# Performance work log

Measured on AMD Instinct MI355X. Metric: run time of the kernel, lower is better.

Reference implementation:

```python
import jax, jax.numpy as jnp
import numpy as np

B, L, IN_DIM, D_MODEL = 4, 1024, 128, 256
MDIM = 2 * D_MODEL          # mamba_dim = 512 (must equal 2*d_model for shape consistency)
NL = 4                      # mamba_layers
DIN = 2 * MDIM              # d_inner (expand=2)
NST = 16                    # d_state
DTR = MDIM // 16            # dt_rank = 32
KC = 4                      # d_conv
EPS = 1e-5

# sinusoidal positional encoding buffer (deterministic)
_pos = np.arange(L, dtype=np.float32)[:, None]
_div = np.exp(np.arange(0, MDIM, 2, dtype=np.float32) * (-np.log(10000.0) / MDIM))
_pe = np.zeros((L, MDIM), dtype=np.float32)
_pe[:, 0::2] = np.sin(_pos * _div)
_pe[:, 1::2] = np.cos(_pos * _div)
PE = jnp.asarray(_pe)


def setup_inputs() -> dict:
    key = jax.random.key(0)
    ks = iter(jax.random.split(key, 64))
    rn = lambda shape, s=0.02: jax.random.normal(next(ks), shape, jnp.float32) * s
    inp = {
        "x": jax.random.normal(next(ks), (B, L, IN_DIM), jnp.float32),
        "rtg": jax.random.normal(next(ks), (B, L, 1), jnp.float32),
        "state_emb_w": rn((D_MODEL, IN_DIM)), "state_emb_b": jnp.zeros((D_MODEL,)),
        "reward_emb_w": rn((D_MODEL, 1)), "reward_emb_b": jnp.zeros((D_MODEL,)),
        "ln_w": jnp.ones((MDIM,)), "ln_b": jnp.zeros((MDIM,)),
        "in_proj_w": rn((NL, 2 * DIN, MDIM)),
        "conv_w": rn((NL, DIN, KC), 0.1), "conv_b": jnp.zeros((NL, DIN)),
        "x_proj_w": rn((NL, DTR + 2 * NST, DIN)),
        "dt_proj_w": rn((NL, DIN, DTR), 0.1), "dt_proj_b": jnp.full((NL, DIN), -2.0),
        "A_log": jnp.tile(jnp.log(jnp.arange(1, NST + 1, dtype=jnp.float32)), (NL, DIN, 1)),
        "D_param": jnp.ones((NL, DIN)),
        "out_proj_w": rn((NL, MDIM, DIN)),
        "norm_w": jnp.ones((NL, MDIM)), "norm_f_w": jnp.ones((MDIM,)),
        "so_w1": rn((MDIM // 2, MDIM)), "so_b1": jnp.zeros((MDIM // 2,)),
        "so_w2": rn((IN_DIM, MDIM // 2)), "so_b2": jnp.zeros((IN_DIM,)),
        "ro_w1": rn((MDIM // 2, MDIM)), "ro_b1": jnp.zeros((MDIM // 2,)),
        "ro_w2": rn((1, MDIM // 2)), "ro_b2": jnp.zeros((1,)),
    }
    return inp


def _rmsnorm(h, w):
    return h * jax.lax.rsqrt(jnp.mean(h * h, -1, keepdims=True) + EPS) * w


def _mamba(h, ipw, cw, cb, xpw, dpw, dpb, Alog, Dp, opw):
    # h: [B,L,MDIM]
    Ls = h.shape[1]
    xz = h @ ipw.T                                   # [B,L,2*DIN]
    xx, z = jnp.split(xz, 2, axis=-1)
    # causal depthwise conv, kernel KC, left pad KC-1
    xp = jnp.pad(xx, ((0, 0), (KC - 1, 0), (0, 0)))
    xc = cb + sum(cw[:, k] * xp[:, k:k + Ls, :] for k in range(KC))
    xc = jax.nn.silu(xc)                             # [B,L,DIN]
    dbc = xc @ xpw.T                                 # [B,L,DTR+2*NST]
    dt = jax.nn.softplus(dbc[..., :DTR] @ dpw.T + dpb)   # [B,L,DIN]
    Bm = dbc[..., DTR:DTR + NST]                     # [B,L,NST]
    Cm = dbc[..., DTR + NST:]                        # [B,L,NST]
    A = -jnp.exp(Alog)                               # [DIN,NST]

    def step(hc, inp):
        dt_t, B_t, C_t, x_t = inp                    # [B,DIN],[B,NST],[B,NST],[B,DIN]
        hc = jnp.exp(dt_t[:, :, None] * A) * hc + (dt_t * x_t)[:, :, None] * B_t[:, None, :]
        return hc, jnp.einsum('bdn,bn->bd', hc, C_t)

    h0 = jnp.zeros((h.shape[0], DIN, NST), h.dtype)
    _, ys = jax.lax.scan(step, h0, (dt.swapaxes(0, 1), Bm.swapaxes(0, 1),
                                    Cm.swapaxes(0, 1), xc.swapaxes(0, 1)))
    y = ys.swapaxes(0, 1) + Dp * xc
    y = y * jax.nn.silu(z)
    return y @ opw.T                                 # [B,L,MDIM]


def _forward(x, rtg, state_emb_w, state_emb_b, reward_emb_w, reward_emb_b, ln_w, ln_b,
             in_proj_w, conv_w, conv_b, x_proj_w, dt_proj_w, dt_proj_b, A_log, D_param,
             out_proj_w, norm_w, norm_f_w, so_w1, so_b1, so_w2, so_b2, ro_w1, ro_b1, ro_w2, ro_b2):
    se = x @ state_emb_w.T + state_emb_b            # [B,L,D_MODEL]
    re = rtg @ reward_emb_w.T + reward_emb_b        # [B,L,D_MODEL]
    h = jnp.concatenate([se, re], axis=-1)          # [B,L,MDIM]
    h = h + PE[:h.shape[1]]                          # dropout is identity at eval
    mu = jnp.mean(h, -1, keepdims=True)
    var = jnp.var(h, -1, keepdims=True)
    h = (h - mu) * jax.lax.rsqrt(var + EPS) * ln_w + ln_b
    residual = None
    for i in range(NL):
        residual = h if residual is None else h + residual
        hn = _rmsnorm(residual, norm_w[i])
        h = _mamba(hn, in_proj_w[i], conv_w[i], conv_b[i], x_proj_w[i],
                   dt_proj_w[i], dt_proj_b[i], A_log[i], D_param[i], out_proj_w[i])
    residual = h + residual
    h = _rmsnorm(residual, norm_f_w)
    next_state = jax.nn.relu(h @ so_w1.T + so_b1) @ so_w2.T + so_b2   # [B,L,IN_DIM]
    next_reward = jax.nn.relu(h @ ro_w1.T + ro_b1) @ ro_w2.T + ro_b2  # [B,L,1]
    return next_state, next_reward


def reference(x, rtg, state_emb_w, state_emb_b, reward_emb_w, reward_emb_b, ln_w, ln_b,
              in_proj_w, conv_w, conv_b, x_proj_w, dt_proj_w, dt_proj_b, A_log, D_param,
              out_proj_w, norm_w, norm_f_w, so_w1, so_b1, so_w2, so_b2, ro_w1, ro_b1, ro_w2, ro_b2):
    return _forward(x, rtg, state_emb_w, state_emb_b, reward_emb_w, reward_emb_b, ln_w, ln_b,
                    in_proj_w, conv_w, conv_b, x_proj_w, dt_proj_w, dt_proj_b, A_log, D_param,
                    out_proj_w, norm_w, norm_f_w, so_w1, so_b1, so_w2, so_b2, ro_w1, ro_b1, ro_w2, ro_b2)
```

## Files before the change

### kernel.cpp

```cpp
#include <hip/hip_runtime.h>
#include <stdint.h>

typedef unsigned short u16;
typedef __attribute__((ext_vector_type(8))) short bf16x8;
typedef __attribute__((ext_vector_type(4))) float f32x4;

static __device__ __forceinline__ u16 f2b(float f) {
  uint32_t u = __builtin_bit_cast(uint32_t, f);
  u += 0x7fffu + ((u >> 16) & 1u);
  return (u16)(u >> 16);
}
static __device__ __forceinline__ float b2f(u16 h) {
  uint32_t u = ((uint32_t)h) << 16;
  return __builtin_bit_cast(float, u);
}

#define GLDS16(gsrc, ldst)                                                        \
  __builtin_amdgcn_global_load_lds(                                               \
      (const __attribute__((address_space(1))) void*)(gsrc),                      \
      (__attribute__((address_space(3))) void*)(ldst), 16, 0, 0)

__global__ void f2b_kernel(const float* __restrict__ in, u16* __restrict__ out, int n) {
  int i = blockIdx.x * 256 + threadIdx.x;
  if (i < n) out[i] = f2b(in[i]);
}

__global__ __launch_bounds__(256) void pe_kernel(float* __restrict__ PEt) {
  const int l = blockIdx.x;
  const float c = -9.210340371976184f / 512.f;
#pragma unroll
  for (int q = 0; q < 2; ++q) {
    int dd = threadIdx.x + q * 256;
    float div = expf((float)(2 * (dd >> 1)) * c);
    float v = (dd & 1) ? cosf((float)l * div) : sinf((float)l * div);
    PEt[(size_t)l * 512 + dd] = v;
  }
}

__global__ __launch_bounds__(256) void dpw_t_kernel(const float* __restrict__ dpw,
                                                    float* __restrict__ dpwT) {
  const int l = blockIdx.y;
  int idx = blockIdx.x * 256 + threadIdx.x;
  int j = idx >> 10, dd = idx & 1023;
  dpwT[(size_t)l * 32768 + idx] = dpw[(size_t)l * 32768 + (size_t)dd * 32 + j];
}

__global__ __launch_bounds__(256) void embed_ln2(
    const float* __restrict__ x, const float* __restrict__ rtg,
    const float* __restrict__ Wse, const float* __restrict__ bse,
    const float* __restrict__ Wre, const float* __restrict__ bre,
    const float* __restrict__ lnw, const float* __restrict__ lnb,
    const float* __restrict__ PEt, float* __restrict__ h) {
  const int tid = threadIdx.x;
  const int tok0 = blockIdx.x * 16;
  const int l0 = tok0 & 1023;
  __shared__ float xs[16][128];
  __shared__ float rt[16];
  __shared__ float sw[16][2][4];
  for (int i = tid; i < 16 * 128; i += 256) ((float*)xs)[i] = x[(size_t)tok0 * 128 + i];
  if (tid < 16) rt[tid] = rtg[tok0 + tid];
  __syncthreads();
  const int d = tid;
  float acc[16];
#pragma unroll
  for (int tt = 0; tt < 16; ++tt) acc[tt] = 0.f;
  const float* wrow = Wse + (size_t)d * 128;
  for (int k0 = 0; k0 < 128; k0 += 8) {
    float4 wa = *(const float4*)(wrow + k0);
    float4 wb = *(const float4*)(wrow + k0 + 4);
#pragma unroll
    for (int tt = 0; tt < 16; ++tt) {
      const float* xr = &xs[tt][k0];
      acc[tt] += xr[0] * wa.x + xr[1] * wa.y + xr[2] * wa.z + xr[3] * wa.w +
                 xr[4] * wb.x + xr[5] * wb.y + xr[6] * wb.z + xr[7] * wb.w;
    }
  }
  const float seb = bse[d], reW = Wre[d], reB = bre[d];
  const int lane = tid & 63, wv = tid >> 6;
  float h1a[16];
#pragma unroll
  for (int tt = 0; tt < 16; ++tt) {
    float h0 = acc[tt] + seb + PEt[(size_t)(l0 + tt) * 512 + d];
    float h1 = reB + rt[tt] * reW + PEt[(size_t)(l0 + tt) * 512 + 256 + d];
    acc[tt] = h0;
    h1a[tt] = h1;
    float s = h0 + h1, q = h0 * h0 + h1 * h1;
#pragma unroll
    for (int o = 32; o; o >>= 1) { s += __shfl_xor(s, o); q += __shfl_xor(q, o); }
    if (lane == 0) { sw[tt][0][wv] = s; sw[tt][1][wv] = q; }
  }
  __syncthreads();
#pragma unroll
  for (int tt = 0; tt < 16; ++tt) {
    float S = sw[tt][0][0] + sw[tt][0][1] + sw[tt][0][2] + sw[tt][0][3];
    float Q = sw[tt][1][0] + sw[tt][1][1] + sw[tt][1][2] + sw[tt][1][3];
    float mean = S * (1.f / 512.f);
    float var = Q * (1.f / 512.f) - mean * mean;
    float rstd = rsqrtf(var + 1e-5f);
    size_t base = (size_t)(tok0 + tt) * 512;
    h[base + d]       = (acc[tt] - mean) * rstd * lnw[d] + lnb[d];
    h[base + 256 + d] = (h1a[tt] - mean) * rstd * lnw[256 + d] + lnb[256 + d];
  }
}

__global__ __launch_bounds__(256) void resid_rms_kernel(
    const float* __restrict__ hin, float* __restrict__ residual,
    const float* __restrict__ w, u16* __restrict__ outb, int first) {
  const int tok = blockIdx.x;
  const int t = threadIdx.x;
  __shared__ float rq[4];
  size_t base = (size_t)tok * 512;
  float v0 = hin[base + t], v1 = hin[base + t + 256];
  if (!first) { v0 += residual[base + t]; v1 += residual[base + t + 256]; }
  residual[base + t] = v0;
  residual[base + t + 256] = v1;
  float q = v0 * v0 + v1 * v1;
#pragma unroll
  for (int o = 32; o; o >>= 1) q += __shfl_xor(q, o);
  if ((t & 63) == 0) rq[t >> 6] = q;
  __syncthreads();
  float Q = rq[0] + rq[1] + rq[2] + rq[3];
  float scale = rsqrtf(Q * (1.f / 512.f) + 1e-5f);
  outb[base + t]       = f2b(v0 * scale * w[t]);
  outb[base + t + 256] = f2b(v1 * scale * w[t + 256]);
}

template <int BM, int BN, int WM, int WN, int EPI>
__global__ __launch_bounds__(256) void gemm_bt(
    const u16* __restrict__ A, const u16* __restrict__ Bw,
    float* __restrict__ Cf, u16* __restrict__ Cb,
    const float* __restrict__ bias, int M, int N, int K) {
  constexpr int MF = BM / (WM * 16);
  constexpr int NF = BN / (WN * 16);
  constexpr int NCA = (BM * 4) / 256;
  constexpr int NCB = (BN * 4) / 256;
  __shared__ __align__(16) u16 lA[BM * 32];
  __shared__ __align__(16) u16 lB[BN * 32];
  const int tid = threadIdx.x;
  const int lane = tid & 63;
  const int wv = tid >> 6;
  const int wr = wv / WN, wc = wv % WN;
  const int m0 = blockIdx.x * BM, n0 = blockIdx.y * BN;
  const int kchunk = K / gridDim.z;
  const int kb = blockIdx.z * kchunk;

  f32x4 acc[MF][NF];
#pragma unroll
  for (int i = 0; i < MF; ++i)
#pragma unroll
    for (int j = 0; j < NF; ++j) acc[i][j] = (f32x4){0.f, 0.f, 0.f, 0.f};

  const int srow = tid >> 2, sck = tid & 3;
  const u16* Ag = A + (size_t)(m0 + srow) * K + sck * 8 + kb;
  const u16* Bg = Bw + (size_t)(n0 + srow) * K + sck * 8 + kb;

  for (int k0 = 0; k0 < kchunk; k0 += 32) {
#pragma unroll
    for (int it = 0; it < NCA; ++it)
      GLDS16(Ag + (size_t)it * 64 * K + k0, &lA[(it * 256 + tid) * 8]);
#pragma unroll
    for (int it = 0; it < NCB; ++it)
      GLDS16(Bg + (size_t)it * 64 * K + k0, &lB[(it * 256 + tid) * 8]);
    __syncthreads();
    bf16x8 af[MF], bfr[NF];
    const int koff = (lane >> 4) * 8;
#pragma unroll
    for (int mi = 0; mi < MF; ++mi) {
      int r = wr * (MF * 16) + mi * 16 + (lane & 15);
      af[mi] = *(const bf16x8*)(&lA[r * 32 + koff]);
    }
#pragma unroll
    for (int ni = 0; ni < NF; ++ni) {
      int r = wc * (NF * 16) + ni * 16 + (lane & 15);
      bfr[ni] = *(const bf16x8*)(&lB[r * 32 + koff]);
    }
#pragma unroll
    for (int mi = 0; mi < MF; ++mi)
#pragma unroll
      for (int ni = 0; ni < NF; ++ni)
        acc[mi][ni] = __builtin_amdgcn_mfma_f32_16x16x32_bf16(af[mi], bfr[ni], acc[mi][ni], 0, 0, 0);
    __syncthreads();
  }

  float* co = Cf + (size_t)blockIdx.z * (size_t)M * N;
  const int rbase = (lane >> 4) * 4;
  const int cbase = lane & 15;
#pragma unroll
  for (int mi = 0; mi < MF; ++mi) {
#pragma unroll
    for (int ni = 0; ni < NF; ++ni) {
      int row = m0 + wr * (MF * 16) + mi * 16 + rbase;
      int col = n0 + wc * (NF * 16) + ni * 16 + cbase;
      float bv = (EPI >= 2) ? bias[col] : 0.f;
#pragma unroll
      for (int r = 0; r < 4; ++r) {
        float v = acc[mi][ni][r] + bv;
        if (EPI == 2) v = fmaxf(v, 0.f);
        size_t idx = (size_t)(row + r) * N + col;
        if (EPI == 1 || EPI == 2) Cb[idx] = f2b(v);
        else co[idx] = v;
      }
    }
  }
}

__global__ __launch_bounds__(256) void conv_silu_kernel(
    const u16* __restrict__ xz, const float* __restrict__ cw,
    const float* __restrict__ cb, float* __restrict__ xc, u16* __restrict__ xcb) {
  int idx = blockIdx.x * 256 + threadIdx.x;
  int d = idx & 1023;
  int t = (idx >> 10) & 1023;
  int token = idx >> 10;
  float4 w4 = *(const float4*)(cw + (size_t)d * 4);
  const float wk[4] = {w4.x, w4.y, w4.z, w4.w};
  float s = cb[d];
  const u16* xx = xz + (size_t)(token - t) * 2048 + d;
#pragma unroll
  for (int k = 0; k < 4; ++k) {
    int tt = t - 3 + k;
    if (tt >= 0) s += wk[k] * b2f(xx[(size_t)tt * 2048]);
  }
  float sl = s / (1.f + expf(-s));
  xc[idx] = sl;
  xcb[idx] = f2b(sl);
}

__global__ __launch_bounds__(256) void dt_kernel2(
    const float* __restrict__ P, const float* __restrict__ dpwT,
    const float* __restrict__ dpb, float* __restrict__ dtout,
    float* __restrict__ dbcr) {
  const int tid = threadIdx.x;
  const int tok0 = blockIdx.x * 16;
  __shared__ float sm[16][64];
  const size_t str = (size_t)4096 * 64;
  for (int i = tid; i < 16 * 64; i += 256) {
    size_t o = (size_t)tok0 * 64 + i;
    float v = P[o] + P[str + o] + P[2 * str + o] + P[3 * str + o];
    ((float*)sm)[i] = v;
    dbcr[o] = v;
  }
  __syncthreads();
  float acc0[16], acc1[16], acc2[16], acc3[16];
#pragma unroll
  for (int t = 0; t < 16; ++t) { acc0[t] = 0.f; acc1[t] = 0.f; acc2[t] = 0.f; acc3[t] = 0.f; }
#pragma unroll 4
  for (int j = 0; j < 32; ++j) {
    float w0 = dpwT[(size_t)j * 1024 + tid];
    float w1 = dpwT[(size_t)j * 1024 + 256 + tid];
    float w2 = dpwT[(size_t)j * 1024 + 512 + tid];
    float w3 = dpwT[(size_t)j * 1024 + 768 + tid];
#pragma unroll
    for (int t = 0; t < 16; ++t) {
      float sv = sm[t][j];
      acc0[t] += sv * w0;
      acc1[t] += sv * w1;
      acc2[t] += sv * w2;
      acc3[t] += sv * w3;
    }
  }
  const float b0 = dpb[tid], b1 = dpb[256 + tid], b2 = dpb[512 + tid], b3 = dpb[768 + tid];
#pragma unroll
  for (int t = 0; t < 16; ++t) {
    size_t o = (size_t)(tok0 + t) * 1024 + tid;
    float a0 = acc0[t] + b0, a1 = acc1[t] + b1, a2 = acc2[t] + b2, a3 = acc3[t] + b3;
    dtout[o]       = (a0 > 20.f) ? a0 : logf(1.f + expf(a0));
    dtout[o + 256] = (a1 > 20.f) ? a1 : logf(1.f + expf(a1));
    dtout[o + 512] = (a2 > 20.f) ? a2 : logf(1.f + expf(a2));
    dtout[o + 768] = (a3 > 20.f) ? a3 : logf(1.f + expf(a3));
  }
}

__global__ __launch_bounds__(256) void scan1(
    const float* __restrict__ dt, const float* __restrict__ xc,
    const float* __restrict__ dbc, const float* __restrict__ Alog,
    float* __restrict__ Ebuf, float* __restrict__ Ubuf, int NCc, int TCc) {
  const int d = blockIdx.x * 256 + threadIdx.x;
  const int c = blockIdx.y;
  const int b = blockIdx.z;
  const int t0 = c * TCc;
  __shared__ __align__(16) float sB[64][16];
  for (int i = threadIdx.x; i < TCc * 16; i += 256) {
    int t = i >> 4, n = i & 15;
    sB[t][n] = dbc[((size_t)(b * 1024 + t0 + t)) * 64 + 32 + n];
  }
  float A2[16];
#pragma unroll
  for (int q = 0; q < 4; ++q) {
    float4 a4 = *(const float4*)(Alog + (size_t)d * 16 + q * 4);
    A2[q * 4 + 0] = -expf(a4.x) * 1.4426950408889634f;
    A2[q * 4 + 1] = -expf(a4.y) * 1.4426950408889634f;
    A2[q * 4 + 2] = -expf(a4.z) * 1.4426950408889634f;
    A2[q * 4 + 3] = -expf(a4.w) * 1.4426950408889634f;
  }
  __syncthreads();
  float hc[16];
#pragma unroll
  for (int n = 0; n < 16; ++n) hc[n] = 0.f;
  float sumdt = 0.f;
  size_t tok = (size_t)b * 1024 + t0;
  for (int t = 0; t < TCc; ++t, ++tok) {
    float dtv = dt[tok * 1024 + d];
    float xcv = xc[tok * 1024 + d];
    float du = dtv * xcv;
    sumdt += dtv;
#pragma unroll
    for (int q = 0; q < 4; ++q) {
      float4 B4 = *(const float4*)(&sB[t][q * 4]);
      float e0 = exp2f(dtv * A2[q * 4 + 0]);
      float e1 = exp2f(dtv * A2[q * 4 + 1]);
      float e2 = exp2f(dtv * A2[q * 4 + 2]);
      float e3 = exp2f(dtv * A2[q * 4 + 3]);
      hc[q * 4 + 0] = e0 * hc[q * 4 + 0] + du * B4.x;
      hc[q * 4 + 1] = e1 * hc[q * 4 + 1] + du * B4.y;
      hc[q * 4 + 2] = e2 * hc[q * 4 + 2] + du * B4.z;
      hc[q * 4 + 3] = e3 * hc[q * 4 + 3] + du * B4.w;
    }
  }
  size_t ob = (((size_t)b * NCc + c) * 16) * 1024 + d;
#pragma unroll
  for (int n = 0; n < 16; ++n) {
    Ebuf[ob + (size_t)n * 1024] = exp2f(A2[n] * sumdt);
    Ubuf[ob + (size_t)n * 1024] = hc[n];
  }
}

__global__ __launch_bounds__(256) void scan_mid(
    const float* __restrict__ Ebuf, const float* __restrict__ Ubuf,
    float* __restrict__ H0, int NCc) {
  int idx = blockIdx.x * 256 + threadIdx.x;
  int b = idx >> 14;
  int nd = idx & 16383;
  float h = 0.f;
  size_t o0 = ((size_t)b * NCc * 16) * 1024 + nd;
  const size_t cstr = (size_t)16 * 1024;
  for (int cc = 0; cc < NCc; ++cc) {
    size_t o = o0 + (size_t)cc * cstr;
    H0[o] = h;
    if (cc < NCc - 1) h = Ebuf[o] * h + Ubuf[o];
  }
}

__global__ __launch_bounds__(256) void scan2(
    const float* __restrict__ dt, const float* __restrict__ xc,
    const float* __restrict__ dbc, const u16* __restrict__ xz,
    const float* __restrict__ Alog, const float* __restrict__ Dp,
    const float* __restrict__ H0, u16* __restrict__ yg, int NCc, int TCc) {
  const int d = blockIdx.x * 256 + threadIdx.x;
  const int c = blockIdx.y;
  const int b = blockIdx.z;
  const int t0 = c * TCc;
  __shared__ __align__(16) float sB[64][16];
  __shared__ __align__(16) float sC[64][16];
  for (int i = threadIdx.x; i < TCc * 16; i += 256) {
    int t = i >> 4, n = i & 15;
    size_t o = ((size_t)(b * 1024 + t0 + t)) * 64 + 32;
    sB[t][n] = dbc[o + n];
    sC[t][n] = dbc[o + 16 + n];
  }
  float A2[16];
#pragma unroll
  for (int q = 0; q < 4; ++q) {
    float4 a4 = *(const float4*)(Alog + (size_t)d * 16 + q * 4);
    A2[q * 4 + 0] = -expf(a4.x) * 1.4426950408889634f;
    A2[q * 4 + 1] = -expf(a4.y) * 1.4426950408889634f;
    A2[q * 4 + 2] = -expf(a4.z) * 1.4426950408889634f;
    A2[q * 4 + 3] = -expf(a4.w) * 1.4426950408889634f;
  }
  const float Dd = Dp[d];
  float hc[16];
  size_t ob = (((size_t)b * NCc + c) * 16) * 1024 + d;
#pragma unroll
  for (int n = 0; n < 16; ++n) hc[n] = H0[ob + (size_t)n * 1024];
  __syncthreads();
  size_t tok = (size_t)b * 1024 + t0;
  for (int t = 0; t < TCc; ++t, ++tok) {
    float dtv = dt[tok * 1024 + d];
    float xcv = xc[tok * 1024 + d];
    float du = dtv * xcv;
    float y0 = 0.f, y1 = 0.f, y2 = 0.f, y3 = 0.f;
#pragma unroll
    for (int q = 0; q < 4; ++q) {
      float4 B4 = *(const float4*)(&sB[t][q * 4]);
      float4 C4 = *(const float4*)(&sC[t][q * 4]);
      float e0 = exp2f(dtv * A2[q * 4 + 0]);
      float e1 = exp2f(dtv * A2[q * 4 + 1]);
      float e2 = exp2f(dtv * A2[q * 4 + 2]);
      float e3 = exp2f(dtv * A2[q * 4 + 3]);
      hc[q * 4 + 0] = e0 * hc[q * 4 + 0] + du * B4.x;
      hc[q * 4 + 1] = e1 * hc[q * 4 + 1] + du * B4.y;
      hc[q * 4 + 2] = e2 * hc[q * 4 + 2] + du * B4.z;
      hc[q * 4 + 3] = e3 * hc[q * 4 + 3] + du * B4.w;
      y0 += hc[q * 4 + 0] * C4.x;
      y1 += hc[q * 4 + 1] * C4.y;
      y2 += hc[q * 4 + 2] * C4.z;
      y3 += hc[q * 4 + 3] * C4.w;
    }
    float y = (y0 + y1) + (y2 + y3);
    float z = b2f(xz[tok * 2048 + 1024 + d]);
    float g = z / (1.f + expf(-z));
    yg[tok * 1024 + d] = f2b((y + Dd * xcv) * g);
  }
}

__global__ __launch_bounds__(256) void reward_head_kernel(
    const u16* __restrict__ t1r, const float* __restrict__ w2,
    const float* __restrict__ b2, float* __restrict__ outr) {
  int tok = blockIdx.x * 4 + (threadIdx.x >> 6);
  int lane = threadIdx.x & 63;
  float s = 0.f;
#pragma unroll
  for (int j = 0; j < 256; j += 64) s += b2f(t1r[(size_t)tok * 256 + j + lane]) * w2[j + lane];
#pragma unroll
  for (int o = 32; o; o >>= 1) s += __shfl_xor(s, o);
  if (lane == 0) outr[tok] = s + b2[0];
}

extern "C" void kernel_launch(void* const* d_in, const int* in_sizes, int n_in,
                              void* d_out, int out_size, void* d_ws, size_t ws_size,
                              hipStream_t stream) {
  const float* x    = (const float*)d_in[0];
  const float* rtg  = (const float*)d_in[1];
  const float* Wse  = (const float*)d_in[2];
  const float* bse  = (const float*)d_in[3];
  const float* Wre  = (const float*)d_in[4];
  const float* bre  = (const float*)d_in[5];
  const float* lnw  = (const float*)d_in[6];
  const float* lnb  = (const float*)d_in[7];
  const float* ipw  = (const float*)d_in[8];
  const float* cw   = (const float*)d_in[9];
  const float* cb   = (const float*)d_in[10];
  const float* xpw  = (const float*)d_in[11];
  const float* dpw  = (const float*)d_in[12];
  const float* dpb  = (const float*)d_in[13];
  const float* Alog = (const float*)d_in[14];
  const float* Dp   = (const float*)d_in[15];
  const float* opw  = (const float*)d_in[16];
  const float* nw   = (const float*)d_in[17];
  const float* nfw  = (const float*)d_in[18];
  const float* sow1 = (const float*)d_in[19];
  const float* sob1 = (const float*)d_in[20];
  const float* sow2 = (const float*)d_in[21];
  const float* sob2 = (const float*)d_in[22];
  const float* row1 = (const float*)d_in[23];
  const float* rob1 = (const float*)d_in[24];
  const float* row2 = (const float*)d_in[25];
  const float* rob2 = (const float*)d_in[26];
  (void)in_sizes; (void)n_in; (void)out_size;

  char* wsp = (char*)d_ws;
  size_t off = 0;
  auto alloc = [&](size_t bytes) -> void* {
    off = (off + 255) & ~(size_t)255;
    void* p = wsp + off;
    off += bytes;
    return p;
  };
  const int TOK = 4096;
  float* h     = (float*)alloc((size_t)TOK * 512 * 4);
  float* resid = (float*)alloc((size_t)TOK * 512 * 4);
  u16* hn      = (u16*)alloc((size_t)TOK * 512 * 2);
  u16* xzb     = (u16*)alloc((size_t)TOK * 2048 * 2);
  float* xcf   = (float*)alloc((size_t)TOK * 1024 * 4);
  u16* xcb     = (u16*)alloc((size_t)TOK * 1024 * 2);
  float* dbcP  = (float*)alloc((size_t)4 * TOK * 64 * 4);
  float* dbc   = (float*)alloc((size_t)TOK * 64 * 4);
  float* dtf   = (float*)alloc((size_t)TOK * 1024 * 4);
  float* PEt   = (float*)alloc((size_t)1024 * 512 * 4);
  float* dpwT  = (float*)alloc((size_t)4 * 32 * 1024 * 4);
  u16* ipwb    = (u16*)alloc((size_t)4 * 2048 * 512 * 2);
  u16* xpwb    = (u16*)alloc((size_t)4 * 64 * 1024 * 2);
  u16* opwb    = (u16*)alloc((size_t)4 * 512 * 1024 * 2);
  u16* sow1b   = (u16*)alloc((size_t)256 * 512 * 2);
  u16* sow2b   = (u16*)alloc((size_t)128 * 256 * 2);
  u16* row1b   = (u16*)alloc((size_t)256 * 512 * 2);

  size_t base_off = (off + 255) & ~(size_t)255;
  auto scan_bytes = [](int nc) {
    return (size_t)3 * 4 * nc * 16 * 1024 * 4 + 512;
  };
  int NCc = 16;
  if (ws_size >= base_off + scan_bytes(64)) NCc = 64;
  else if (ws_size >= base_off + scan_bytes(32)) NCc = 32;
  int TCc = 1024 / NCc;
  char* shared8 = (char*)alloc((size_t)2 * 4096 * NCc * 16 * 4);
  float* Ebuf  = (float*)shared8;
  float* Ubuf  = Ebuf + (size_t)4096 * NCc * 16;
  float* H0    = (float*)alloc((size_t)4096 * NCc * 16 * 4);
  u16* t1s     = (u16*)shared8;
  u16* t1r     = t1s + (size_t)TOK * 256;

  auto cvt = [&](const float* src, u16* dst, int n) {
    f2b_kernel<<<(n + 255) / 256, 256, 0, stream>>>(src, dst, n);
  };
  cvt(ipw, ipwb, 4 * 2048 * 512);
  cvt(xpw, xpwb, 4 * 64 * 1024);
  cvt(opw, opwb, 4 * 512 * 1024);
  cvt(sow1, sow1b, 256 * 512);
  cvt(sow2, sow2b, 128 * 256);
  cvt(row1, row1b, 256 * 512);

  pe_kernel<<<1024, 256, 0, stream>>>(PEt);
  dpw_t_kernel<<<dim3(128, 4), 256, 0, stream>>>(dpw, dpwT);
  embed_ln2<<<256, 256, 0, stream>>>(x, rtg, Wse, bse, Wre, bre, lnw, lnb, PEt, h);

  for (int i = 0; i < 4; ++i) {
    resid_rms_kernel<<<TOK, 256, 0, stream>>>(h, resid, nw + i * 512, hn, i == 0);
    gemm_bt<128, 128, 2, 2, 1><<<dim3(32, 16, 1), 256, 0, stream>>>(
        hn, ipwb + (size_t)i * 2048 * 512, nullptr, xzb, nullptr, 4096, 2048, 512);
    conv_silu_kernel<<<TOK * 1024 / 256, 256, 0, stream>>>(
        xzb, cw + (size_t)i * 4096, cb + i * 1024, xcf, xcb);
    gemm_bt<128, 64, 2, 2, 0><<<dim3(32, 1, 4), 256, 0, stream>>>(
        xcb, xpwb + (size_t)i * 64 * 1024, dbcP, nullptr, nullptr, 4096, 64, 1024);
    dt_kernel2<<<TOK / 16, 256, 0, stream>>>(dbcP, dpwT + (size_t)i * 32 * 1024,
                                             dpb + i * 1024, dtf, dbc);
    scan1<<<dim3(4, NCc - 1, 4), 256, 0, stream>>>(
        dtf, xcf, dbc, Alog + (size_t)i * 1024 * 16, Ebuf, Ubuf, NCc, TCc);
    scan_mid<<<256, 256, 0, stream>>>(Ebuf, Ubuf, H0, NCc);
    scan2<<<dim3(4, NCc, 4), 256, 0, stream>>>(
        dtf, xcf, dbc, xzb, Alog + (size_t)i * 1024 * 16, Dp + i * 1024,
        H0, xcb, NCc, TCc);
    gemm_bt<128, 64, 2, 2, 0><<<dim3(32, 8, 1), 256, 0, stream>>>(
        xcb, opwb + (size_t)i * 512 * 1024, h, nullptr, nullptr, 4096, 512, 1024);
  }

  resid_rms_kernel<<<TOK, 256, 0, stream>>>(h, resid, nfw, hn, 0);
  gemm_bt<64, 64, 2, 2, 2><<<dim3(64, 4, 1), 256, 0, stream>>>(
      hn, sow1b, nullptr, t1s, sob1, 4096, 256, 512);
  gemm_bt<64, 64, 2, 2, 3><<<dim3(64, 2, 1), 256, 0, stream>>>(
      t1s, sow2b, (float*)d_out, nullptr, sob2, 4096, 128, 256);
  gemm_bt<64, 64, 2, 2, 2><<<dim3(64, 4, 1), 256, 0, stream>>>(
      hn, row1b, nullptr, t1r, rob1, 4096, 256, 512);
  reward_head_kernel<<<TOK / 4, 256, 0, stream>>>(
      t1r, row2, rob2, (float*)d_out + (size_t)TOK * 128);
}
```

Before: 721.0 us.

## Merge setup launches, vectorize conv-SiLU, fuse both head first-layer GEMMs

Folds the six weight conversions, the PE table, the dt_proj transpose and a new conv-weight transpose into one setup kernel, removing about eight launches. The depthwise conv+SiLU now handles 8 channels per thread with vector loads and stores, using transposed conv weights. The state and reward head first-layer GEMMs become a single N=512 GEMM that relies on sow1b and row1b being allocated next to each other, with a strided-A parameter added so the second head GEMM can read its half. This saves launches and memory traffic, but the setup kernel branches a lot and the fused GEMM depends on that adjacent allocation.

```diff
diff --git a/kernel.cpp b/kernel.cpp
--- a/kernel.cpp
+++ b/kernel.cpp
@@ -3,6 +3,7 @@
 
 typedef unsigned short u16;
 typedef __attribute__((ext_vector_type(8))) short bf16x8;
+typedef __attribute__((ext_vector_type(8))) u16 u16x8;
 typedef __attribute__((ext_vector_type(4))) float f32x4;
 
 static __device__ __forceinline__ u16 f2b(float f) {
@@ -20,29 +21,39 @@
       (const __attribute__((address_space(1))) void*)(gsrc),                      \
       (__attribute__((address_space(3))) void*)(ldst), 16, 0, 0)
 
-__global__ void f2b_kernel(const float* __restrict__ in, u16* __restrict__ out, int n) {
+__global__ __launch_bounds__(256) void setup_kernel(
+    const float* __restrict__ ipw, u16* __restrict__ ipwb,
+    const float* __restrict__ xpw, u16* __restrict__ xpwb,
+    const float* __restrict__ opw, u16* __restrict__ opwb,
+    const float* __restrict__ sow1, u16* __restrict__ sow1b,
+    const float* __restrict__ sow2, u16* __restrict__ sow2b,
+    const float* __restrict__ row1, u16* __restrict__ row1b,
+    float* __restrict__ PEt,
+    const float* __restrict__ dpw, float* __restrict__ dpwT,
+    const float* __restrict__ cw, float* __restrict__ cwT) {
   int i = blockIdx.x * 256 + threadIdx.x;
-  if (i < n) out[i] = f2b(in[i]);
-}
-
-__global__ __launch_bounds__(256) void pe_kernel(float* __restrict__ PEt) {
-  const int l = blockIdx.x;
-  const float c = -9.210340371976184f / 512.f;
-#pragma unroll
-  for (int q = 0; q < 2; ++q) {
-    int dd = threadIdx.x + q * 256;
-    float div = expf((float)(2 * (dd >> 1)) * c);
-    float v = (dd & 1) ? cosf((float)l * div) : sinf((float)l * div);
-    PEt[(size_t)l * 512 + dd] = v;
-  }
-}
-
-__global__ __launch_bounds__(256) void dpw_t_kernel(const float* __restrict__ dpw,
-                                                    float* __restrict__ dpwT) {
-  const int l = blockIdx.y;
-  int idx = blockIdx.x * 256 + threadIdx.x;
-  int j = idx >> 10, dd = idx & 1023;
-  dpwT[(size_t)l * 32768 + idx] = dpw[(size_t)l * 32768 + (size_t)dd * 32 + j];
+  if (i < 4194304) { ipwb[i] = f2b(ipw[i]); return; } i -= 4194304;
+  if (i < 262144)  { xpwb[i] = f2b(xpw[i]); return; } i -= 262144;
+  if (i < 2097152) { opwb[i] = f2b(opw[i]); return; } i -= 2097152;
+  if (i < 131072)  { sow1b[i] = f2b(sow1[i]); return; } i -= 131072;
+  if (i < 32768)   { sow2b[i] = f2b(sow2[i]); return; } i -= 32768;
+  if (i < 131072)  { row1b[i] = f2b(row1[i]); return; } i -= 131072;
+  if (i < 524288) {
+    int dd = i & 511, l = i >> 9;
+    const float cc = -9.210340371976184f / 512.f;
+    float div = expf((float)(2 * (dd >> 1)) * cc);
+    PEt[i] = (dd & 1) ? cosf((float)l * div) : sinf((float)l * div);
+    return;
+  } i -= 524288;
+  if (i < 131072) {
+    int l = i >> 15, r = i & 32767, j = r >> 10, dd = r & 1023;
+    dpwT[i] = dpw[(size_t)l * 32768 + (size_t)dd * 32 + j];
+    return;
+  } i -= 131072;
+  if (i < 16384) {
+    int l = i >> 12, r = i & 4095, k = r >> 10, dd = r & 1023;
+    cwT[i] = cw[(size_t)l * 4096 + (size_t)dd * 4 + k];
+  }
 }
 
 __global__ __launch_bounds__(256) void embed_ln2(
@@ -129,7 +140,8 @@
 __global__ __launch_bounds__(256) void gemm_bt(
     const u16* __restrict__ A, const u16* __restrict__ Bw,
     float* __restrict__ Cf, u16* __restrict__ Cb,
-    const float* __restrict__ bias, int M, int N, int K) {
+    const float* __restrict__ bias, const float* __restrict__ bias2,
+    int M, int N, int K, int As) {
   constexpr int MF = BM / (WM * 16);
   constexpr int NF = BN / (WN * 16);
   constexpr int NCA = (BM * 4) / 256;
@@ -151,13 +163,13 @@
     for (int j = 0; j < NF; ++j) acc[i][j] = (f32x4){0.f, 0.f, 0.f, 0.f};
 
   const int srow = tid >> 2, sck = tid & 3;
-  const u16* Ag = A + (size_t)(m0 + srow) * K + sck * 8 + kb;
+  const u16* Ag = A + (size_t)(m0 + srow) * As + sck * 8 + kb;
   const u16* Bg = Bw + (size_t)(n0 + srow) * K + sck * 8 + kb;
 
   for (int k0 = 0; k0 < kchunk; k0 += 32) {
 #pragma unroll
     for (int it = 0; it < NCA; ++it)
-      GLDS16(Ag + (size_t)it * 64 * K + k0, &lA[(it * 256 + tid) * 8]);
+      GLDS16(Ag + (size_t)it * 64 * As + k0, &lA[(it * 256 + tid) * 8]);
 #pragma unroll
     for (int it = 0; it < NCB; ++it)
       GLDS16(Bg + (size_t)it * 64 * K + k0, &lB[(it * 256 + tid) * 8]);
@@ -191,38 +203,62 @@
     for (int ni = 0; ni < NF; ++ni) {
       int row = m0 + wr * (MF * 16) + mi * 16 + rbase;
       int col = n0 + wc * (NF * 16) + ni * 16 + cbase;
-      float bv = (EPI >= 2) ? bias[col] : 0.f;
+      float bv = 0.f;
+      if (EPI == 2 || EPI == 3) bv = bias[col];
+      if (EPI == 4) bv = (col < 256) ? bias[col] : bias2[col - 256];
 #pragma unroll
       for (int r = 0; r < 4; ++r) {
         float v = acc[mi][ni][r] + bv;
-        if (EPI == 2) v = fmaxf(v, 0.f);
+        if (EPI == 2 || EPI == 4) v = fmaxf(v, 0.f);
         size_t idx = (size_t)(row + r) * N + col;
-        if (EPI == 1 || EPI == 2) Cb[idx] = f2b(v);
+        if (EPI == 1 || EPI == 2 || EPI == 4) Cb[idx] = f2b(v);
         else co[idx] = v;
       }
     }
   }
 }
 
-__global__ __launch_bounds__(256) void conv_silu_kernel(
-    const u16* __restrict__ xz, const float* __restrict__ cw,
-    const float* __restrict__ cb, float* __restrict__ xc, u16* __restrict__ xcb) {
-  int idx = blockIdx.x * 256 + threadIdx.x;
-  int d = idx & 1023;
-  int t = (idx >> 10) & 1023;
-  int token = idx >> 10;
-  float4 w4 = *(const float4*)(cw + (size_t)d * 4);
-  const float wk[4] = {w4.x, w4.y, w4.z, w4.w};
-  float s = cb[d];
-  const u16* xx = xz + (size_t)(token - t) * 2048 + d;
+__global__ __launch_bounds__(256) void conv_silu_f(
+    const u16* __restrict__ xz, const float* __restrict__ cwT,
+    const float* __restrict__ cb, float* __restrict__ xcf, u16* __restrict__ xcb) {
+  int gid = blockIdx.x * 256 + threadIdx.x;
+  int d0 = (gid & 127) * 8;
+  int token = gid >> 7;
+  int t = token & 1023;
+  const u16* xx = xz + (size_t)(token - t) * 2048 + d0;
+  float s[8];
+  {
+    float4 cba = *(const float4*)(cb + d0);
+    float4 cbb = *(const float4*)(cb + d0 + 4);
+    s[0] = cba.x; s[1] = cba.y; s[2] = cba.z; s[3] = cba.w;
+    s[4] = cbb.x; s[5] = cbb.y; s[6] = cbb.z; s[7] = cbb.w;
+  }
 #pragma unroll
   for (int k = 0; k < 4; ++k) {
     int tt = t - 3 + k;
-    if (tt >= 0) s += wk[k] * b2f(xx[(size_t)tt * 2048]);
-  }
-  float sl = s / (1.f + expf(-s));
-  xc[idx] = sl;
-  xcb[idx] = f2b(sl);
+    if (tt >= 0) {
+      u16x8 v = *(const u16x8*)(xx + (size_t)tt * 2048);
+      float4 wA = *(const float4*)(cwT + (size_t)k * 1024 + d0);
+      float4 wB = *(const float4*)(cwT + (size_t)k * 1024 + d0 + 4);
+      s[0] += wA.x * b2f(v[0]); s[1] += wA.y * b2f(v[1]);
+      s[2] += wA.z * b2f(v[2]); s[3] += wA.w * b2f(v[3]);
+      s[4] += wB.x * b2f(v[4]); s[5] += wB.y * b2f(v[5]);
+      s[6] += wB.z * b2f(v[6]); s[7] += wB.w * b2f(v[7]);
+    }
+  }
+  u16x8 o;
+  float4 fa, fb;
+#pragma unroll
+  for (int j = 0; j < 8; ++j) {
+    float sl = s[j] / (1.f + expf(-s[j]));
+    s[j] = sl;
+    o[j] = f2b(sl);
+  }
+  fa.x = s[0]; fa.y = s[1]; fa.z = s[2]; fa.w = s[3];
+  fb.x = s[4]; fb.y = s[5]; fb.z = s[6]; fb.w = s[7];
+  *(float4*)(xcf + (size_t)token * 1024 + d0) = fa;
+  *(float4*)(xcf + (size_t)token * 1024 + d0 + 4) = fb;
+  *(u16x8*)(xcb + (size_t)token * 1024 + d0) = o;
 }
 
 __global__ __launch_bounds__(256) void dt_kernel2(
@@ -403,13 +439,14 @@
 }
 
 __global__ __launch_bounds__(256) void reward_head_kernel(
-    const u16* __restrict__ t1r, const float* __restrict__ w2,
+    const u16* __restrict__ t1sr, const float* __restrict__ w2,
     const float* __restrict__ b2, float* __restrict__ outr) {
   int tok = blockIdx.x * 4 + (threadIdx.x >> 6);
   int lane = threadIdx.x & 63;
   float s = 0.f;
 #pragma unroll
-  for (int j = 0; j < 256; j += 64) s += b2f(t1r[(size_t)tok * 256 + j + lane]) * w2[j + lane];
+  for (int j = 0; j < 256; j += 64)
+    s += b2f(t1sr[(size_t)tok * 512 + 256 + j + lane]) * w2[j + lane];
 #pragma unroll
   for (int o = 32; o; o >>= 1) s += __shfl_xor(s, o);
   if (lane == 0) outr[tok] = s + b2[0];
@@ -467,12 +504,13 @@
   float* dtf   = (float*)alloc((size_t)TOK * 1024 * 4);
   float* PEt   = (float*)alloc((size_t)1024 * 512 * 4);
   float* dpwT  = (float*)alloc((size_t)4 * 32 * 1024 * 4);
+  float* cwT   = (float*)alloc((size_t)4 * 4 * 1024 * 4);
   u16* ipwb    = (u16*)alloc((size_t)4 * 2048 * 512 * 2);
   u16* xpwb    = (u16*)alloc((size_t)4 * 64 * 1024 * 2);
   u16* opwb    = (u16*)alloc((size_t)4 * 512 * 1024 * 2);
   u16* sow1b   = (u16*)alloc((size_t)256 * 512 * 2);
+  u16* row1b   = (u16*)alloc((size_t)256 * 512 * 2);
   u16* sow2b   = (u16*)alloc((size_t)128 * 256 * 2);
-  u16* row1b   = (u16*)alloc((size_t)256 * 512 * 2);
 
   size_t base_off = (off + 255) & ~(size_t)255;
   auto scan_bytes = [](int nc) {
@@ -486,31 +524,23 @@
   float* Ebuf  = (float*)shared8;
   float* Ubuf  = Ebuf + (size_t)4096 * NCc * 16;
   float* H0    = (float*)alloc((size_t)4096 * NCc * 16 * 4);
-  u16* t1s     = (u16*)shared8;
-  u16* t1r     = t1s + (size_t)TOK * 256;
-
-  auto cvt = [&](const float* src, u16* dst, int n) {
-    f2b_kernel<<<(n + 255) / 256, 256, 0, stream>>>(src, dst, n);
-  };
-  cvt(ipw, ipwb, 4 * 2048 * 512);
-  cvt(xpw, xpwb, 4 * 64 * 1024);
-  cvt(opw, opwb, 4 * 512 * 1024);
-  cvt(sow1, sow1b, 256 * 512);
-  cvt(sow2, sow2b, 128 * 256);
-  cvt(row1, row1b, 256 * 512);
-
-  pe_kernel<<<1024, 256, 0, stream>>>(PEt);
-  dpw_t_kernel<<<dim3(128, 4), 256, 0, stream>>>(dpw, dpwT);
+  u16* t1sr    = (u16*)shared8;
+
+  setup_kernel<<<29376, 256, 0, stream>>>(ipw, ipwb, xpw, xpwb, opw, opwb,
+                                          sow1, sow1b, sow2, sow2b, row1, row1b,
+                                          PEt, dpw, dpwT, cw, cwT);
   embed_ln2<<<256, 256, 0, stream>>>(x, rtg, Wse, bse, Wre, bre, lnw, lnb, PEt, h);
 
   for (int i = 0; i < 4; ++i) {
     resid_rms_kernel<<<TOK, 256, 0, stream>>>(h, resid, nw + i * 512, hn, i == 0);
     gemm_bt<128, 128, 2, 2, 1><<<dim3(32, 16, 1), 256, 0, stream>>>(
-        hn, ipwb + (size_t)i * 2048 * 512, nullptr, xzb, nullptr, 4096, 2048, 512);
-    conv_silu_kernel<<<TOK * 1024 / 256, 256, 0, stream>>>(
-        xzb, cw + (size_t)i * 4096, cb + i * 1024, xcf, xcb);
+        hn, ipwb + (size_t)i * 2048 * 512, nullptr, xzb, nullptr, nullptr,
+        4096, 2048, 512, 512);
+    conv_silu_f<<<2048, 256, 0, stream>>>(
+        xzb, cwT + (size_t)i * 4096, cb + i * 1024, xcf, xcb);
     gemm_bt<128, 64, 2, 2, 0><<<dim3(32, 1, 4), 256, 0, stream>>>(
-        xcb, xpwb + (size_t)i * 64 * 1024, dbcP, nullptr, nullptr, 4096, 64, 1024);
+        xcb, xpwb + (size_t)i * 64 * 1024, dbcP, nullptr, nullptr, nullptr,
+        4096, 64, 1024, 1024);
     dt_kernel2<<<TOK / 16, 256, 0, stream>>>(dbcP, dpwT + (size_t)i * 32 * 1024,
                                              dpb + i * 1024, dtf, dbc);
     scan1<<<dim3(4, NCc - 1, 4), 256, 0, stream>>>(
@@ -520,16 +550,15 @@
         dtf, xcf, dbc, xzb, Alog + (size_t)i * 1024 * 16, Dp + i * 1024,
         H0, xcb, NCc, TCc);
     gemm_bt<128, 64, 2, 2, 0><<<dim3(32, 8, 1), 256, 0, stream>>>(
-        xcb, opwb + (size_t)i * 512 * 1024, h, nullptr, nullptr, 4096, 512, 1024);
+        xcb, opwb + (size_t)i * 512 * 1024, h, nullptr, nullptr, nullptr,
+        4096, 512, 1024, 1024);
   }
 
   resid_rms_kernel<<<TOK, 256, 0, stream>>>(h, resid, nfw, hn, 0);
-  gemm_bt<64, 64, 2, 2, 2><<<dim3(64, 4, 1), 256, 0, stream>>>(
-      hn, sow1b, nullptr, t1s, sob1, 4096, 256, 512);
+  gemm_bt<64, 64, 2, 2, 4><<<dim3(64, 8, 1), 256, 0, stream>>>(
+      hn, sow1b, nullptr, t1sr, sob1, rob1, 4096, 512, 512, 512);
   gemm_bt<64, 64, 2, 2, 3><<<dim3(64, 2, 1), 256, 0, stream>>>(
-      t1s, sow2b, (float*)d_out, nullptr, sob2, 4096, 128, 256);
-  gemm_bt<64, 64, 2, 2, 2><<<dim3(64, 4, 1), 256, 0, stream>>>(
-      hn, row1b, nullptr, t1r, rob1, 4096, 256, 512);
+      t1sr, sow2b, (float*)d_out, nullptr, sob2, nullptr, 4096, 128, 256, 512);
   reward_head_kernel<<<TOK / 4, 256, 0, stream>>>(
-      t1r, row2, rob2, (float*)d_out + (size_t)TOK * 128);
-}
+      t1sr, row2, rob2, (float*)d_out + (size_t)TOK * 128);
+}
```

After: 673.0 us, median of 2. 1.07x faster.
